# Performance work log

Measured on AMD Instinct MI355X. Metric: run time of the kernel, lower is better.

## Reference

```python
import jax, jax.numpy as jnp
import numpy as np

BATCH = 4096
TEMP = 0.5
EPS = 1e-12  # torch F.normalize eps

def setup_inputs() -> dict:
    key = jax.random.key(0)
    k1, k2 = jax.random.split(key)
    z_i = jax.random.normal(k1, (BATCH, 256), dtype=jnp.float32)
    z_j = jax.random.normal(k2, (BATCH, 256), dtype=jnp.float32)
    return {"z_i": z_i, "z_j": z_j}

def _l2norm(x):
    n = jnp.sqrt(jnp.sum(x * x, axis=1, keepdims=True))
    return x / jnp.maximum(n, EPS)

def reference(z_i, z_j):
    B = z_i.shape[0]
    zi = _l2norm(z_i)
    zj = _l2norm(z_j)
    reps = jnp.concatenate([zi, zj], axis=0)          # [2B, D]
    # rows are unit-norm, so cosine similarity == dot product (GEMM)
    sim = reps @ reps.T                                # [2B, 2B]
    sim_ij = jnp.diagonal(sim, offset=B)               # [B]
    sim_ji = jnp.diagonal(sim, offset=-B)              # [B]
    positives = jnp.concatenate([sim_ij, sim_ji], 0)   # [2B]
    nominator = jnp.exp(positives / TEMP)
    # negatives_mask: ones with the two same-view BxB diagonal blocks zeroed
    idx = jnp.arange(2 * B)
    half = (idx >= B).astype(sim.dtype)                # 0 for first half, 1 for second
    mask = (half[:, None] != half[None, :]).astype(sim.dtype)  # cross-view blocks = 1
    denom = jnp.sum(mask * jnp.exp(sim / TEMP), axis=1)
    loss_partial = -jnp.log(nominator / denom)
    return jnp.sum(loss_partial) / (2 * B)
```

## Files before the change

kernel.cpp:

```cpp
#include <hip/hip_runtime.h>
#include <hip/hip_bf16.h>

#define BATCH 4096
#define DIM 256

typedef __attribute__((ext_vector_type(8))) short short8;
typedef __attribute__((ext_vector_type(4))) float f32x4;

__device__ inline unsigned short f2bf(float f) {
    union { float f; unsigned u; } x; x.f = f;
    unsigned r = x.u + 0x7fffu + ((x.u >> 16) & 1u);
    return (unsigned short)(r >> 16);
}

#define WS_FAST_BYTES ((size_t)4 * 1024 * 1024 + 3 * 4096 * sizeof(float) + 64)

__device__ inline short8* lds8(unsigned short* base, int r, int c) {
    int byte = (r << 7) + (c << 1);
    byte ^= (r & 7) << 4;
    return reinterpret_cast<short8*>(reinterpret_cast<char*>(base) + byte);
}

__global__ __launch_bounds__(256) void norm2_kernel(
    const float* __restrict__ zi, const float* __restrict__ zj,
    unsigned short* __restrict__ zib, unsigned short* __restrict__ zjb,
    float* __restrict__ pos, float* __restrict__ rowsum, float* __restrict__ colsum,
    float* __restrict__ tmp, int* __restrict__ counter) {
    const int tid = threadIdx.x;
    if (blockIdx.x < 16) rowsum[blockIdx.x * 256 + tid] = 0.f;
    else if (blockIdx.x < 32) colsum[(blockIdx.x - 16) * 256 + tid] = 0.f;
    else if (blockIdx.x == 32 && tid == 0) { tmp[0] = 0.f; *counter = 0; }

    const int wid  = tid >> 6;
    const int lane = tid & 63;
    const int row  = blockIdx.x * 4 + wid;
    const float4 vi = reinterpret_cast<const float4*>(zi)[row * 64 + lane];
    const float4 vj = reinterpret_cast<const float4*>(zj)[row * 64 + lane];
    float si = vi.x * vi.x + vi.y * vi.y + vi.z * vi.z + vi.w * vi.w;
    float sj = vj.x * vj.x + vj.y * vj.y + vj.z * vj.z + vj.w * vj.w;
    float d  = vi.x * vj.x + vi.y * vj.y + vi.z * vj.z + vi.w * vj.w;
#pragma unroll
    for (int o = 1; o < 64; o <<= 1) {
        si += __shfl_xor(si, o);
        sj += __shfl_xor(sj, o);
        d  += __shfl_xor(d, o);
    }
    const float ii = 1.0f / fmaxf(sqrtf(si), 1e-12f);
    const float ij = 1.0f / fmaxf(sqrtf(sj), 1e-12f);
    ushort4 a = make_ushort4(f2bf(vi.x * ii), f2bf(vi.y * ii), f2bf(vi.z * ii), f2bf(vi.w * ii));
    ushort4 b = make_ushort4(f2bf(vj.x * ij), f2bf(vj.y * ij), f2bf(vj.z * ij), f2bf(vj.w * ij));
    reinterpret_cast<ushort4*>(zib)[row * 64 + lane] = a;
    reinterpret_cast<ushort4*>(zjb)[row * 64 + lane] = b;
    if (lane == 0) pos[row] = d * ii * ij;
}

__global__ __launch_bounds__(256) void sim128_kernel(
    const unsigned short* __restrict__ zib, const unsigned short* __restrict__ zjb,
    float* __restrict__ rowsum, float* __restrict__ colsum) {
    __shared__ unsigned short As[2][128 * 64];
    __shared__ unsigned short Bs[2][128 * 64];
    const int wg = blockIdx.x + (blockIdx.y << 5);
    const int bi = ((wg & 7) << 2) + ((wg >> 3) & 3);
    const int bj = wg >> 5;
    const int tid  = threadIdx.x;
    const int wave = tid >> 6;
    const int lane = tid & 63;
    const int wr = (wave >> 1) << 6;
    const int wc = (wave & 1) << 6;
    const int fr = lane & 15;
    const int ko = (lane >> 4) << 3;

    const unsigned short* gA = zib + (size_t)bi * 128 * DIM;
    const unsigned short* gB = zjb + (size_t)bj * 128 * DIM;
    int rr[4], cc[4];
#pragma unroll
    for (int i = 0; i < 4; ++i) {
        int chunk = i * 256 + tid;
        rr[i] = chunk >> 3;
        cc[i] = (chunk & 7) << 3;
    }

    short8 pa[4], pb[4];
#pragma unroll
    for (int i = 0; i < 4; ++i) {
        pa[i] = *reinterpret_cast<const short8*>(gA + rr[i] * DIM + cc[i]);
        pb[i] = *reinterpret_cast<const short8*>(gB + rr[i] * DIM + cc[i]);
    }
#pragma unroll
    for (int i = 0; i < 4; ++i) {
        *lds8(As[0], rr[i], cc[i]) = pa[i];
        *lds8(Bs[0], rr[i], cc[i]) = pb[i];
    }

    f32x4 acc[4][4] = {};

#pragma unroll
    for (int s = 0; s < 4; ++s) {
        const int cur = s & 1;
        __syncthreads();
        if (s < 3) {
#pragma unroll
            for (int i = 0; i < 4; ++i) {
                pa[i] = *reinterpret_cast<const short8*>(gA + rr[i] * DIM + (s + 1) * 64 + cc[i]);
                pb[i] = *reinterpret_cast<const short8*>(gB + rr[i] * DIM + (s + 1) * 64 + cc[i]);
            }
        }
#pragma unroll
        for (int kk = 0; kk < 2; ++kk) {
            int c = kk * 32 + ko;
            short8 a0 = *lds8(As[cur], wr +      fr, c);
            short8 a1 = *lds8(As[cur], wr + 16 + fr, c);
            short8 a2 = *lds8(As[cur], wr + 32 + fr, c);
            short8 a3 = *lds8(As[cur], wr + 48 + fr, c);
            short8 b0 = *lds8(Bs[cur], wc +      fr, c);
            short8 b1 = *lds8(Bs[cur], wc + 16 + fr, c);
            short8 b2 = *lds8(Bs[cur], wc + 32 + fr, c);
            short8 b3 = *lds8(Bs[cur], wc + 48 + fr, c);
            acc[0][0] = __builtin_amdgcn_mfma_f32_16x16x32_bf16(a0, b0, acc[0][0], 0, 0, 0);
            acc[0][1] = __builtin_amdgcn_mfma_f32_16x16x32_bf16(a0, b1, acc[0][1], 0, 0, 0);
            acc[0][2] = __builtin_amdgcn_mfma_f32_16x16x32_bf16(a0, b2, acc[0][2], 0, 0, 0);
            acc[0][3] = __builtin_amdgcn_mfma_f32_16x16x32_bf16(a0, b3, acc[0][3], 0, 0, 0);
            acc[1][0] = __builtin_amdgcn_mfma_f32_16x16x32_bf16(a1, b0, acc[1][0], 0, 0, 0);
            acc[1][1] = __builtin_amdgcn_mfma_f32_16x16x32_bf16(a1, b1, acc[1][1], 0, 0, 0);
            acc[1][2] = __builtin_amdgcn_mfma_f32_16x16x32_bf16(a1, b2, acc[1][2], 0, 0, 0);
            acc[1][3] = __builtin_amdgcn_mfma_f32_16x16x32_bf16(a1, b3, acc[1][3], 0, 0, 0);
            acc[2][0] = __builtin_amdgcn_mfma_f32_16x16x32_bf16(a2, b0, acc[2][0], 0, 0, 0);
            acc[2][1] = __builtin_amdgcn_mfma_f32_16x16x32_bf16(a2, b1, acc[2][1], 0, 0, 0);
            acc[2][2] = __builtin_amdgcn_mfma_f32_16x16x32_bf16(a2, b2, acc[2][2], 0, 0, 0);
            acc[2][3] = __builtin_amdgcn_mfma_f32_16x16x32_bf16(a2, b3, acc[2][3], 0, 0, 0);
            acc[3][0] = __builtin_amdgcn_mfma_f32_16x16x32_bf16(a3, b0, acc[3][0], 0, 0, 0);
            acc[3][1] = __builtin_amdgcn_mfma_f32_16x16x32_bf16(a3, b1, acc[3][1], 0, 0, 0);
            acc[3][2] = __builtin_amdgcn_mfma_f32_16x16x32_bf16(a3, b2, acc[3][2], 0, 0, 0);
            acc[3][3] = __builtin_amdgcn_mfma_f32_16x16x32_bf16(a3, b3, acc[3][3], 0, 0, 0);
        }
        if (s < 3) {
#pragma unroll
            for (int i = 0; i < 4; ++i) {
                *lds8(As[cur ^ 1], rr[i], cc[i]) = pa[i];
                *lds8(Bs[cur ^ 1], rr[i], cc[i]) = pb[i];
            }
        }
    }

    const float SC = 2.0f * 1.44269504088896f;
    float rs[4][4];
#pragma unroll
    for (int m = 0; m < 4; ++m)
#pragma unroll
        for (int r = 0; r < 4; ++r) rs[m][r] = 0.f;
    float cs[4] = {0.f, 0.f, 0.f, 0.f};
#pragma unroll
    for (int m = 0; m < 4; ++m)
#pragma unroll
        for (int n = 0; n < 4; ++n)
#pragma unroll
            for (int r = 0; r < 4; ++r) {
                float e = exp2f(acc[m][n][r] * SC);
                rs[m][r] += e;
                cs[n] += e;
            }

#pragma unroll
    for (int m = 0; m < 4; ++m)
#pragma unroll
        for (int r = 0; r < 4; ++r) {
            float v = rs[m][r];
            v += __shfl_xor(v, 1); v += __shfl_xor(v, 2);
            v += __shfl_xor(v, 4); v += __shfl_xor(v, 8);
            if ((lane & 15) == 0) {
                int row = bi * 128 + wr + m * 16 + (lane >> 4) * 4 + r;
                atomicAdd(&rowsum[row], v);
            }
        }
#pragma unroll
    for (int n = 0; n < 4; ++n) {
        float v = cs[n];
        v += __shfl_xor(v, 16); v += __shfl_xor(v, 32);
        if (lane < 16) atomicAdd(&colsum[bj * 128 + wc + n * 16 + lane], v);
    }
}

__global__ __launch_bounds__(256) void loss2_kernel(
    const float* __restrict__ rowsum, const float* __restrict__ colsum,
    const float* __restrict__ pos, float* __restrict__ tmp,
    int* __restrict__ counter, float* __restrict__ out) {
    const int b = blockIdx.x;
    const int tid = threadIdx.x;
    const int idx = (b & 15) * 256 + tid;
    float a = (b < 16) ? (__logf(rowsum[idx]) - 4.0f * pos[idx])
                       : __logf(colsum[idx]);
#pragma unroll
    for (int o = 1; o < 64; o <<= 1) a += __shfl_xor(a, o);
    __shared__ float red[4];
    if ((tid & 63) == 0) red[tid >> 6] = a;
    __syncthreads();
    if (tid == 0) {
        float p = red[0] + red[1] + red[2] + red[3];
        atomicAdd(tmp, p);
        __threadfence();
        int t = atomicAdd(counter, 1);
        if (t == 31) {
            float tot = atomicAdd(tmp, 0.0f);
            out[0] = tot * (1.0f / (2.0f * BATCH));
        }
    }
}

__device__ inline short8* ldsp128(unsigned short* base, int r, int c) {
    int byte = (r << 8) + (c << 1);
    byte ^= (r & 7) << 4;
    return reinterpret_cast<short8*>(reinterpret_cast<char*>(base) + byte);
}

__global__ __launch_bounds__(256) void init_kernel(float* __restrict__ rowsum,
                                                   float* __restrict__ colsum) {
    int i = blockIdx.x * 256 + threadIdx.x;
    rowsum[i] = 0.f;
    colsum[i] = 0.f;
}

__global__ __launch_bounds__(256) void norm_kernel(
    const float* __restrict__ zi, const float* __restrict__ zj,
    float* __restrict__ ninv_i, float* __restrict__ ninv_j, float* __restrict__ pos) {
    const int wid  = threadIdx.x >> 6;
    const int lane = threadIdx.x & 63;
    const int row  = blockIdx.x * 4 + wid;
    const float4 vi = reinterpret_cast<const float4*>(zi)[row * 64 + lane];
    const float4 vj = reinterpret_cast<const float4*>(zj)[row * 64 + lane];
    float si = vi.x * vi.x + vi.y * vi.y + vi.z * vi.z + vi.w * vi.w;
    float sj = vj.x * vj.x + vj.y * vj.y + vj.z * vj.z + vj.w * vj.w;
    float d  = vi.x * vj.x + vi.y * vj.y + vi.z * vj.z + vi.w * vj.w;
#pragma unroll
    for (int o = 1; o < 64; o <<= 1) {
        si += __shfl_xor(si, o);
        sj += __shfl_xor(sj, o);
        d  += __shfl_xor(d, o);
    }
    if (lane == 0) {
        float ii = 1.0f / fmaxf(sqrtf(si), 1e-12f);
        float ij = 1.0f / fmaxf(sqrtf(sj), 1e-12f);
        ninv_i[row] = ii;
        ninv_j[row] = ij;
        pos[row] = d * ii * ij;
    }
}

__global__ __launch_bounds__(256) void sim_kernel(
    const float* __restrict__ zi, const float* __restrict__ zj,
    const float* __restrict__ ninv_i, const float* __restrict__ ninv_j,
    float* __restrict__ rowsum, float* __restrict__ colsum) {
    __shared__ unsigned short As[64 * 128];
    __shared__ unsigned short Bs[64 * 128];
    const int bi = blockIdx.x, bj = blockIdx.y;
    const int tid  = threadIdx.x;
    const int wave = tid >> 6;
    const int lane = tid & 63;
    const int wr = (wave >> 1) << 5;
    const int wc = (wave & 1) << 5;
    const int fr = lane & 15;
    const int ko = (lane >> 4) << 3;

    f32x4 acc[2][2] = {};

    for (int h = 0; h < 2; ++h) {
#pragma unroll
        for (int it = 0; it < 4; ++it) {
            int chunk = tid + it * 256;
            int r = chunk >> 4;
            int c = (chunk & 15) << 3;
            int ga = bi * 64 + r;
            int gb = bj * 64 + r;
            int cgl = h * 128 + c;
            const float4* pa = reinterpret_cast<const float4*>(zi) + ga * 64 + (cgl >> 2);
            const float4* pb = reinterpret_cast<const float4*>(zj) + gb * 64 + (cgl >> 2);
            float4 a0 = pa[0], a1 = pa[1];
            float4 b0 = pb[0], b1 = pb[1];
            float ia = ninv_i[ga];
            float ib = ninv_j[gb];
            short8 va, vb;
            va[0] = (short)f2bf(a0.x * ia); va[1] = (short)f2bf(a0.y * ia);
            va[2] = (short)f2bf(a0.z * ia); va[3] = (short)f2bf(a0.w * ia);
            va[4] = (short)f2bf(a1.x * ia); va[5] = (short)f2bf(a1.y * ia);
            va[6] = (short)f2bf(a1.z * ia); va[7] = (short)f2bf(a1.w * ia);
            vb[0] = (short)f2bf(b0.x * ib); vb[1] = (short)f2bf(b0.y * ib);
            vb[2] = (short)f2bf(b0.z * ib); vb[3] = (short)f2bf(b0.w * ib);
            vb[4] = (short)f2bf(b1.x * ib); vb[5] = (short)f2bf(b1.y * ib);
            vb[6] = (short)f2bf(b1.z * ib); vb[7] = (short)f2bf(b1.w * ib);
            *ldsp128(As, r, c) = va;
            *ldsp128(Bs, r, c) = vb;
        }
        __syncthreads();
#pragma unroll
        for (int kk = 0; kk < 4; ++kk) {
            int c = kk * 32 + ko;
            short8 a0 = *ldsp128(As, wr + fr, c);
            short8 a1 = *ldsp128(As, wr + 16 + fr, c);
            short8 b0 = *ldsp128(Bs, wc + fr, c);
            short8 b1 = *ldsp128(Bs, wc + 16 + fr, c);
            acc[0][0] = __builtin_amdgcn_mfma_f32_16x16x32_bf16(a0, b0, acc[0][0], 0, 0, 0);
            acc[0][1] = __builtin_amdgcn_mfma_f32_16x16x32_bf16(a0, b1, acc[0][1], 0, 0, 0);
            acc[1][0] = __builtin_amdgcn_mfma_f32_16x16x32_bf16(a1, b0, acc[1][0], 0, 0, 0);
            acc[1][1] = __builtin_amdgcn_mfma_f32_16x16x32_bf16(a1, b1, acc[1][1], 0, 0, 0);
        }
        __syncthreads();
    }

    const float SC = 2.0f * 1.44269504088896f;
    float rs[2][4];
#pragma unroll
    for (int m = 0; m < 2; ++m)
#pragma unroll
        for (int r = 0; r < 4; ++r) rs[m][r] = 0.f;
    float cs[2] = {0.f, 0.f};
#pragma unroll
    for (int m = 0; m < 2; ++m)
#pragma unroll
        for (int n = 0; n < 2; ++n)
#pragma unroll
            for (int r = 0; r < 4; ++r) {
                float e = exp2f(acc[m][n][r] * SC);
                rs[m][r] += e;
                cs[n] += e;
            }
#pragma unroll
    for (int m = 0; m < 2; ++m)
#pragma unroll
        for (int r = 0; r < 4; ++r) {
            float v = rs[m][r];
            v += __shfl_xor(v, 1); v += __shfl_xor(v, 2);
            v += __shfl_xor(v, 4); v += __shfl_xor(v, 8);
            if ((lane & 15) == 0) {
                int row = bi * 64 + wr + m * 16 + (lane >> 4) * 4 + r;
                atomicAdd(&rowsum[row], v);
            }
        }
#pragma unroll
    for (int n = 0; n < 2; ++n) {
        float v = cs[n];
        v += __shfl_xor(v, 16); v += __shfl_xor(v, 32);
        if (lane < 16) atomicAdd(&colsum[bj * 64 + wc + n * 16 + lane], v);
    }
}

__global__ __launch_bounds__(256) void loss_kernel(
    const float* __restrict__ rowsum, const float* __restrict__ colsum,
    const float* __restrict__ pos, float* __restrict__ out) {
    float a = 0.f;
    for (int i = threadIdx.x; i < BATCH; i += 256)
        a += __logf(rowsum[i]) + __logf(colsum[i]) - 4.0f * pos[i];
#pragma unroll
    for (int o = 1; o < 64; o <<= 1) a += __shfl_xor(a, o);
    __shared__ float red[4];
    if ((threadIdx.x & 63) == 0) red[threadIdx.x >> 6] = a;
    __syncthreads();
    if (threadIdx.x == 0) {
        float t = red[0] + red[1] + red[2] + red[3];
        out[0] = t * (1.0f / (2.0f * BATCH));
    }
}

extern "C" void kernel_launch(void* const* d_in, const int* in_sizes, int n_in,
                              void* d_out, int out_size, void* d_ws, size_t ws_size,
                              hipStream_t stream) {
    const float* zi = (const float*)d_in[0];
    const float* zj = (const float*)d_in[1];
    char* ws = (char*)d_ws;

    if (ws_size >= WS_FAST_BYTES) {
        unsigned short* zib = (unsigned short*)ws;
        unsigned short* zjb = (unsigned short*)(ws + (size_t)2 * 1024 * 1024);
        float* pos    = (float*)(ws + (size_t)4 * 1024 * 1024);
        float* rowsum = pos + 4096;
        float* colsum = rowsum + 4096;
        float* tmp    = colsum + 4096;
        int*   counter = (int*)(tmp + 1);
        norm2_kernel<<<BATCH / 4, 256, 0, stream>>>(zi, zj, zib, zjb, pos, rowsum, colsum, tmp, counter);
        dim3 grid(32, 32);
        sim128_kernel<<<grid, 256, 0, stream>>>(zib, zjb, rowsum, colsum);
        loss2_kernel<<<32, 256, 0, stream>>>(rowsum, colsum, pos, tmp, counter, (float*)d_out);
    } else {
        float* wsf = (float*)ws;
        float* ninv_i = wsf;
        float* ninv_j = wsf + 4096;
        float* pos    = wsf + 8192;
        float* rowsum = wsf + 12288;
        float* colsum = wsf + 16384;
        init_kernel<<<16, 256, 0, stream>>>(rowsum, colsum);
        norm_kernel<<<BATCH / 4, 256, 0, stream>>>(zi, zj, ninv_i, ninv_j, pos);
        dim3 grid(64, 64);
        sim_kernel<<<grid, 256, 0, stream>>>(zi, zj, ninv_i, ninv_j, rowsum, colsum);
        loss_kernel<<<1, 256, 0, stream>>>(rowsum, colsum, pos, (float*)d_out);
    }
}
```

Measured before the change: 33.51 us.

## Compute two column tiles per workgroup reusing A rows and overlapping epilogue

Each workgroup now processes two 128x128 similarity tiles that share the same A row block, halving the grid to 512 blocks. The first tile's exp/reduction/atomic epilogue runs inside the software-pipelined k-loop, so global loads for the second tile are in flight during it. This aims to amortize block startup, reuse row-tile scheduling, and hide epilogue latency, at the cost of fewer resident waves and higher register pressure.

```diff
diff --git a/kernel.cpp b/kernel.cpp
--- a/kernel.cpp
+++ b/kernel.cpp
@@ -54,14 +54,12 @@
     if (lane == 0) pos[row] = d * ii * ij;
 }
 
-__global__ __launch_bounds__(256) void sim128_kernel(
+__global__ __launch_bounds__(256) void sim2_kernel(
     const unsigned short* __restrict__ zib, const unsigned short* __restrict__ zjb,
     float* __restrict__ rowsum, float* __restrict__ colsum) {
     __shared__ unsigned short As[2][128 * 64];
     __shared__ unsigned short Bs[2][128 * 64];
-    const int wg = blockIdx.x + (blockIdx.y << 5);
-    const int bi = ((wg & 7) << 2) + ((wg >> 3) & 3);
-    const int bj = wg >> 5;
+    const int b    = blockIdx.x;
     const int tid  = threadIdx.x;
     const int wave = tid >> 6;
     const int lane = tid & 63;
@@ -70,8 +68,13 @@
     const int fr = lane & 15;
     const int ko = (lane >> 4) << 3;
 
-    const unsigned short* gA = zib + (size_t)bi * 128 * DIM;
-    const unsigned short* gB = zjb + (size_t)bj * 128 * DIM;
+    const int bi  = ((b & 7) << 2) + ((b >> 3) & 3);
+    const int bj0 = b >> 5;
+    const int bj1 = bj0 + 16;
+    const unsigned short* gA  = zib + (size_t)bi  * 128 * DIM;
+    const unsigned short* gB0 = zjb + (size_t)bj0 * 128 * DIM;
+    const unsigned short* gB1 = zjb + (size_t)bj1 * 128 * DIM;
+
     int rr[4], cc[4];
 #pragma unroll
     for (int i = 0; i < 4; ++i) {
@@ -79,12 +82,50 @@
         rr[i] = chunk >> 3;
         cc[i] = (chunk & 7) << 3;
     }
+    const float SC = 2.0f * 1.44269504088896f;
+
+    auto epilogue = [&](f32x4 (&acc)[4][4], int bjx) {
+        float rs[4][4];
+#pragma unroll
+        for (int m = 0; m < 4; ++m)
+#pragma unroll
+            for (int r = 0; r < 4; ++r) rs[m][r] = 0.f;
+        float csn[4] = {0.f, 0.f, 0.f, 0.f};
+#pragma unroll
+        for (int m = 0; m < 4; ++m)
+#pragma unroll
+            for (int n = 0; n < 4; ++n)
+#pragma unroll
+                for (int r = 0; r < 4; ++r) {
+                    float e = exp2f(acc[m][n][r] * SC);
+                    rs[m][r] += e;
+                    csn[n] += e;
+                }
+#pragma unroll
+        for (int m = 0; m < 4; ++m)
+#pragma unroll
+            for (int r = 0; r < 4; ++r) {
+                float v = rs[m][r];
+                v += __shfl_xor(v, 1); v += __shfl_xor(v, 2);
+                v += __shfl_xor(v, 4); v += __shfl_xor(v, 8);
+                if ((lane & 15) == 0) {
+                    int row = bi * 128 + wr + m * 16 + (lane >> 4) * 4 + r;
+                    atomicAdd(&rowsum[row], v);
+                }
+            }
+#pragma unroll
+        for (int n = 0; n < 4; ++n) {
+            float v = csn[n];
+            v += __shfl_xor(v, 16); v += __shfl_xor(v, 32);
+            if (lane < 16) atomicAdd(&colsum[bjx * 128 + wc + n * 16 + lane], v);
+        }
+    };
 
     short8 pa[4], pb[4];
 #pragma unroll
     for (int i = 0; i < 4; ++i) {
-        pa[i] = *reinterpret_cast<const short8*>(gA + rr[i] * DIM + cc[i]);
-        pb[i] = *reinterpret_cast<const short8*>(gB + rr[i] * DIM + cc[i]);
+        pa[i] = *reinterpret_cast<const short8*>(gA  + rr[i] * DIM + cc[i]);
+        pb[i] = *reinterpret_cast<const short8*>(gB0 + rr[i] * DIM + cc[i]);
     }
 #pragma unroll
     for (int i = 0; i < 4; ++i) {
@@ -95,14 +136,17 @@
     f32x4 acc[4][4] = {};
 
 #pragma unroll
-    for (int s = 0; s < 4; ++s) {
-        const int cur = s & 1;
+    for (int p = 0; p < 8; ++p) {
+        const int cur = p & 1;
         __syncthreads();
-        if (s < 3) {
+        if (p < 7) {
+            const int np = p + 1;
+            const int co = (np & 3) * 64;
+            const unsigned short* gBn = (np >> 2) ? gB1 : gB0;
 #pragma unroll
             for (int i = 0; i < 4; ++i) {
-                pa[i] = *reinterpret_cast<const short8*>(gA + rr[i] * DIM + (s + 1) * 64 + cc[i]);
-                pb[i] = *reinterpret_cast<const short8*>(gB + rr[i] * DIM + (s + 1) * 64 + cc[i]);
+                pa[i] = *reinterpret_cast<const short8*>(gA  + rr[i] * DIM + co + cc[i]);
+                pb[i] = *reinterpret_cast<const short8*>(gBn + rr[i] * DIM + co + cc[i]);
             }
         }
 #pragma unroll
@@ -133,7 +177,14 @@
             acc[3][2] = __builtin_amdgcn_mfma_f32_16x16x32_bf16(a3, b2, acc[3][2], 0, 0, 0);
             acc[3][3] = __builtin_amdgcn_mfma_f32_16x16x32_bf16(a3, b3, acc[3][3], 0, 0, 0);
         }
-        if (s < 3) {
+        if (p == 3) {
+            epilogue(acc, bj0);
+#pragma unroll
+            for (int m = 0; m < 4; ++m)
+#pragma unroll
+                for (int n = 0; n < 4; ++n) acc[m][n] = f32x4{0.f, 0.f, 0.f, 0.f};
+        }
+        if (p < 7) {
 #pragma unroll
             for (int i = 0; i < 4; ++i) {
                 *lds8(As[cur ^ 1], rr[i], cc[i]) = pa[i];
@@ -141,43 +192,7 @@
             }
         }
     }
-
-    const float SC = 2.0f * 1.44269504088896f;
-    float rs[4][4];
-#pragma unroll
-    for (int m = 0; m < 4; ++m)
-#pragma unroll
-        for (int r = 0; r < 4; ++r) rs[m][r] = 0.f;
-    float cs[4] = {0.f, 0.f, 0.f, 0.f};
-#pragma unroll
-    for (int m = 0; m < 4; ++m)
-#pragma unroll
-        for (int n = 0; n < 4; ++n)
-#pragma unroll
-            for (int r = 0; r < 4; ++r) {
-                float e = exp2f(acc[m][n][r] * SC);
-                rs[m][r] += e;
-                cs[n] += e;
-            }
-
-#pragma unroll
-    for (int m = 0; m < 4; ++m)
-#pragma unroll
-        for (int r = 0; r < 4; ++r) {
-            float v = rs[m][r];
-            v += __shfl_xor(v, 1); v += __shfl_xor(v, 2);
-            v += __shfl_xor(v, 4); v += __shfl_xor(v, 8);
-            if ((lane & 15) == 0) {
-                int row = bi * 128 + wr + m * 16 + (lane >> 4) * 4 + r;
-                atomicAdd(&rowsum[row], v);
-            }
-        }
-#pragma unroll
-    for (int n = 0; n < 4; ++n) {
-        float v = cs[n];
-        v += __shfl_xor(v, 16); v += __shfl_xor(v, 32);
-        if (lane < 16) atomicAdd(&colsum[bj * 128 + wc + n * 16 + lane], v);
-    }
+    epilogue(acc, bj1);
 }
 
 __global__ __launch_bounds__(256) void loss2_kernel(
@@ -375,8 +390,7 @@
         float* tmp    = colsum + 4096;
         int*   counter = (int*)(tmp + 1);
         norm2_kernel<<<BATCH / 4, 256, 0, stream>>>(zi, zj, zib, zjb, pos, rowsum, colsum, tmp, counter);
-        dim3 grid(32, 32);
-        sim128_kernel<<<grid, 256, 0, stream>>>(zib, zjb, rowsum, colsum);
+        sim2_kernel<<<512, 256, 0, stream>>>(zib, zjb, rowsum, colsum);
         loss2_kernel<<<32, 256, 0, stream>>>(rowsum, colsum, pos, tmp, counter, (float*)d_out);
     } else {
         float* wsf = (float*)ws;
```

Result: faster. 32.54 us (-2.9%).
